# Performance work log

Measured on AMD Instinct MI355X. Metric: run time of the kernel, lower is better.

The kernel has to match this reference:

```python
import jax, jax.numpy as jnp
import numpy as np

DELTA_A, DELTA_R = 0.1, 1.0
ALPHA, BETA, GAMMA = 1.0, 1.0, 0.001


def setup_inputs() -> dict:
    key = jax.random.key(0)
    B, D, H, W, K = 4, 32, 512, 512, 16
    out = jax.random.normal(key, (B, D, H, W), dtype=jnp.float32)
    # 4x4 block partition -> K=16 instance labels, one center per block
    gh, gw = 4, 4
    bh, bw = H // gh, W // gw
    rows = np.arange(H) // bh  # [H]
    cols = np.arange(W) // bw  # [W]
    labels = (rows[:, None] * gw + cols[None, :]).astype(np.int32)  # [H,W]
    target = jnp.asarray(np.broadcast_to(labels, (B, H, W)).copy())
    ctr = np.array([[r * bh + bh // 2, c * bw + bw // 2]
                    for r in range(gh) for c in range(gw)], dtype=np.int32)  # [K,2]
    centers = jnp.asarray(np.broadcast_to(ctr, (B, K, 2)).copy())
    return {"out": out, "target": target, "centers": centers, "batch_size": B}


def _safe_sqrt(x):
    # matches torch.linalg.norm subgradient 0 at 0 (avoids NaN grads)
    pos = x > 0
    return jnp.where(pos, jnp.sqrt(jnp.where(pos, x, 1.0)), 0.0)


def _pairwise_norm(a, b):
    # a [M,D], b [N,D] -> [M,N] euclidean distances via gram trick
    d2 = (jnp.sum(a * a, 1)[:, None] + jnp.sum(b * b, 1)[None, :]
          - 2.0 * a @ b.T)
    return _safe_sqrt(jax.nn.relu(d2))


def _per_image(o, t, c):
    # o [D,H,W], t [H,W] int, c [K,2] int
    D = o.shape[0]
    K = c.shape[0]
    x = o.reshape(D, -1).T                      # [HW, D]
    E = o[:, c[:, 0], c[:, 1]].T                # [K, D] center embeddings
    lab_c = t[c[:, 0], c[:, 1]]                 # [K]
    mask = (t.reshape(-1)[None, :] == lab_c[:, None])  # [K, HW]
    # attraction: hinged distance of every cluster pixel to its center
    norms = _pairwise_norm(E, x)                # [K, HW]
    hinged = jax.nn.relu(norms - DELTA_A) * mask
    cnt = jnp.sum(mask, axis=1)
    denom = jnp.maximum(cnt - 1, 1).astype(o.dtype)
    s_att = jnp.sum(jnp.sum(hinged, axis=1) / denom)
    # repelling: pairwise center distances; diagonal contributes relu(delta_r)
    # per row and the original subtracts delta_r per center -> excluded
    nE = _pairwise_norm(E, E)                   # [K, K]
    s_rep = jnp.sum(jax.nn.relu(DELTA_R - nE)) - K * DELTA_R
    # regularization: norm of each center embedding
    s_reg = jnp.sum(_safe_sqrt(jnp.sum(E * E, axis=1)))
    return s_att, s_rep, s_reg


def reference(out, target, centers, batch_size):
    K = centers.shape[1]
    s_att, s_rep, s_reg = jax.vmap(_per_image)(out, target, centers)  # [B] each
    div_att = jnp.float32(K)
    div_rep = jnp.float32(K * (K - 1))
    div_reg = jnp.float32(K)

    def step(carry, s):
        a, r, g = carry
        sa, sr, sg = s
        return ((a + sa) / div_att, (r + sr) / div_rep, (g + sg) / div_reg), None

    zero = jnp.float32(0.0)
    (att, rep, reg), _ = jax.lax.scan(step, (zero, zero, zero),
                                      (s_att, s_rep, s_reg))
    loss = ALPHA * att + BETA * rep + GAMMA * reg
    return loss, att, rep
```

## Files before the change

kernel.cpp:

```cpp
#include <hip/hip_runtime.h>

#define B_ 4
#define D_ 32
#define H_ 512
#define W_ 512
#define K_ 16
#define N_ (H_ * W_)
#define NQ_ (N_ / 4)
#define NBLK_ 256
#define EPAD 33

#define WS_SUM  0
#define WS_CNT  64
#define WS_E2   128
#define WS_LAB  192
#define WS_E    264
#define WS_PART 4096

typedef float vfloat4 __attribute__((ext_vector_type(4)));
typedef int vint4 __attribute__((ext_vector_type(4)));

__device__ inline vfloat4 nt_load_f4(const float* p) {
  return __builtin_nontemporal_load((const vfloat4*)p);
}
__device__ inline vint4 nt_load_i4(const int* p) {
  return __builtin_nontemporal_load((const vint4*)p);
}

__global__ __launch_bounds__(256) void attract_kernel(
    const float* __restrict__ outp, const int* __restrict__ target,
    const int* __restrict__ centers, float* __restrict__ ws) {
  const int b = blockIdx.y;
  const int tid = threadIdx.x;
  __shared__ float sE[K_ * EPAD];
  __shared__ float se2[K_];
  __shared__ int slab[K_];
  __shared__ int scy[K_], scx[K_];
  __shared__ float bs[K_];
  __shared__ float bc[K_];

  if (tid < 2 * K_) {
    const int v = centers[b * (2 * K_) + tid];
    if (tid & 1) scx[tid >> 1] = v; else scy[tid >> 1] = v;
  }
  __syncthreads();
  {
    const int k = tid >> 4, d0 = tid & 15;
    const size_t cbase = ((size_t)b * D_ * H_ + scy[k]) * W_ + scx[k];
    const float v0 = outp[cbase + (size_t)d0 * N_];
    const float v1 = outp[cbase + (size_t)(d0 + 16) * N_];
    sE[k * EPAD + d0] = v0;
    sE[k * EPAD + d0 + 16] = v1;
    float p = fmaf(v0, v0, v1 * v1);
#pragma unroll
    for (int off = 1; off < 16; off <<= 1) p += __shfl_xor(p, off, 64);
    if (blockIdx.x == 0) {
      ws[WS_E + (b * K_ + k) * D_ + d0] = v0;
      ws[WS_E + (b * K_ + k) * D_ + d0 + 16] = v1;
      if ((tid & 15) == 0) ws[WS_E2 + b * K_ + k] = p;
    }
    if ((tid & 15) == 0) se2[k] = p;
    if (tid < K_) {
      slab[tid] = target[(size_t)b * N_ + scy[tid] * W_ + scx[tid]];
      bs[tid] = 0.0f;
      bc[tid] = 0.0f;
    }
  }
  __syncthreads();

  const int q = blockIdx.x * 256 + tid;
  const float* xb = outp + (size_t)b * D_ * N_;
  const vint4 lab4 = nt_load_i4(target + (size_t)b * N_ + 4 * q);
  const int labv[4] = {lab4.x, lab4.y, lab4.z, lab4.w};

  int kf[4], nm[4];
#pragma unroll
  for (int j = 0; j < 4; ++j) { kf[j] = 0; nm[j] = 0; }
#pragma unroll
  for (int k = 0; k < K_; ++k) {
    const int lk = slab[k];
#pragma unroll
    for (int j = 0; j < 4; ++j) {
      if (labv[j] == lk) { if (nm[j] == 0) kf[j] = k; nm[j]++; }
    }
  }

  float dot[4] = {0.f, 0.f, 0.f, 0.f};
  float x2[4] = {0.f, 0.f, 0.f, 0.f};
#pragma unroll
  for (int d = 0; d < D_; ++d) {
    const vfloat4 x = nt_load_f4(xb + (size_t)d * N_ + 4 * q);
    const float xs[4] = {x.x, x.y, x.z, x.w};
#pragma unroll
    for (int j = 0; j < 4; ++j) {
      const float e = sE[kf[j] * EPAD + d];
      dot[j] = fmaf(xs[j], e, dot[j]);
      x2[j] = fmaf(xs[j], xs[j], x2[j]);
    }
  }

  float hv[4];
#pragma unroll
  for (int j = 0; j < 4; ++j) {
    const float d2 = x2[j] + se2[kf[j]] - 2.0f * dot[j];
    const float h = fmaxf(sqrtf(fmaxf(d2, 0.0f)) - 0.1f, 0.0f);
    hv[j] = (nm[j] > 0) ? h : 0.0f;
  }

  const bool same = (kf[0] == kf[1]) & (kf[1] == kf[2]) & (kf[2] == kf[3]);
  float hsum = hv[0] + hv[1] + hv[2] + hv[3];
  float csum = (float)((nm[0] > 0) + (nm[1] > 0) + (nm[2] > 0) + (nm[3] > 0));
  int gi = same ? (kf[0] + 1) : 0;
#pragma unroll
  for (int off = 1; off < 32; off <<= 1) {
    const int o = __shfl_xor(gi, off, 64);
    if (o != gi) gi = 0;
  }
  if (gi != 0) {
#pragma unroll
    for (int off = 1; off < 32; off <<= 1) {
      hsum += __shfl_xor(hsum, off, 64);
      csum += __shfl_xor(csum, off, 64);
    }
    if ((tid & 31) == 0 && csum > 0.0f) {
      atomicAdd(&bs[gi - 1], hsum);
      atomicAdd(&bc[gi - 1], csum);
    }
  } else if (same) {
    if (csum > 0.0f) {
      atomicAdd(&bs[kf[0]], hsum);
      atomicAdd(&bc[kf[0]], csum);
    }
  } else {
#pragma unroll
    for (int j = 0; j < 4; ++j) {
      if (nm[j] > 0) {
        atomicAdd(&bs[kf[j]], hv[j]);
        atomicAdd(&bc[kf[j]], 1.0f);
      }
    }
  }

  const bool extra = (nm[0] > 1) | (nm[1] > 1) | (nm[2] > 1) | (nm[3] > 1);
  if (__any(extra)) {
    for (int k = 0; k < K_; ++k) {
      bool need[4]; bool anyn = false;
#pragma unroll
      for (int j = 0; j < 4; ++j) {
        need[j] = (nm[j] > 1) && (labv[j] == slab[k]) && (k != kf[j]);
        anyn |= need[j];
      }
      if (__any(anyn)) {
        float dt[4] = {0.f, 0.f, 0.f, 0.f};
        for (int d = 0; d < D_; ++d) {
          const vfloat4 x = nt_load_f4(xb + (size_t)d * N_ + 4 * q);
          const float e = sE[k * EPAD + d];
          dt[0] = fmaf(x.x, e, dt[0]);
          dt[1] = fmaf(x.y, e, dt[1]);
          dt[2] = fmaf(x.z, e, dt[2]);
          dt[3] = fmaf(x.w, e, dt[3]);
        }
#pragma unroll
        for (int j = 0; j < 4; ++j) {
          if (need[j]) {
            const float d2 = x2[j] + se2[k] - 2.0f * dt[j];
            atomicAdd(&bs[k], fmaxf(sqrtf(fmaxf(d2, 0.0f)) - 0.1f, 0.0f));
            atomicAdd(&bc[k], 1.0f);
          }
        }
      }
    }
  }
  __syncthreads();

  if (tid < 2 * K_) {
    float* p = ws + WS_PART + ((size_t)b * NBLK_ + blockIdx.x) * (2 * K_);
    p[tid] = (tid < K_) ? bs[tid] : bc[tid - K_];
  }
}

__global__ __launch_bounds__(256) void final_kernel(const float* __restrict__ ws,
                                                    float* __restrict__ out) {
  const int tid = threadIdx.x;
  __shared__ float sE[B_ * K_ * D_];
  __shared__ float ps[4][64], pc[4][64];
  __shared__ float sred[256];
  __shared__ float srep[B_];
  __shared__ float sreg[B_];
  __shared__ float ssa[B_];

  for (int i = tid; i < B_ * K_ * D_; i += 256) sE[i] = ws[WS_E + i];

  const int pair = tid & 63, quarter = tid >> 6;
  const int pb = pair >> 4, pk = pair & 15;
  {
    const float* base =
        ws + WS_PART + ((size_t)pb * NBLK_ + quarter * 64) * (2 * K_);
    float s = 0.0f, c = 0.0f;
#pragma unroll 4
    for (int i = 0; i < 64; ++i) {
      s += base[i * (2 * K_) + pk];
      c += base[i * (2 * K_) + K_ + pk];
    }
    ps[quarter][pair] = s;
    pc[quarter][pair] = c;
  }
  __syncthreads();

  if (tid < 64) {
    const float s = ps[0][tid] + ps[1][tid] + ps[2][tid] + ps[3][tid];
    const float c = pc[0][tid] + pc[1][tid] + pc[2][tid] + pc[3][tid];
    float v = s / fmaxf(c - 1.0f, 1.0f);
#pragma unroll
    for (int off = 1; off < K_; off <<= 1) v += __shfl_xor(v, off, 64);
    if ((tid & 15) == 0) ssa[tid >> 4] = v;
  }
  __syncthreads();

  const int i = tid >> 4, j = tid & 15;
  for (int b = 0; b < B_; ++b) {
    float dotv = 0.0f;
#pragma unroll 8
    for (int d = 0; d < D_; ++d)
      dotv = fmaf(sE[(b * K_ + i) * D_ + d], sE[(b * K_ + j) * D_ + d], dotv);
    const float d2 = ws[WS_E2 + b * K_ + i] + ws[WS_E2 + b * K_ + j] - 2.0f * dotv;
    sred[tid] = fmaxf(1.0f - sqrtf(fmaxf(d2, 0.0f)), 0.0f);
    __syncthreads();
    for (int s = 128; s > 0; s >>= 1) {
      if (tid < s) sred[tid] += sred[tid + s];
      __syncthreads();
    }
    if (tid == 0) srep[b] = sred[0] - (float)K_;
    __syncthreads();
  }

  sred[tid] = (tid < B_ * K_) ? sqrtf(fmaxf(ws[WS_E2 + tid], 0.0f)) : 0.0f;
  __syncthreads();
  if (tid < B_) {
    float sg = 0.0f;
    for (int k = 0; k < K_; ++k) sg += sred[tid * K_ + k];
    sreg[tid] = sg;
  }
  __syncthreads();

  if (tid == 0) {
    float att = 0.0f, rep = 0.0f, reg = 0.0f;
    for (int b = 0; b < B_; ++b) {
      att = (att + ssa[b]) / (float)K_;
      rep = (rep + srep[b]) / (float)(K_ * (K_ - 1));
      reg = (reg + sreg[b]) / (float)K_;
    }
    out[0] = att + rep + 0.001f * reg;
    out[1] = att;
    out[2] = rep;
  }
}

extern "C" void kernel_launch(void* const* d_in, const int* in_sizes, int n_in,
                              void* d_out, int out_size, void* d_ws, size_t ws_size,
                              hipStream_t stream) {
  const float* outp = (const float*)d_in[0];
  const int* target = (const int*)d_in[1];
  const int* centers = (const int*)d_in[2];
  float* ws = (float*)d_ws;
  float* out = (float*)d_out;

  attract_kernel<<<dim3(NBLK_, B_), 256, 0, stream>>>(outp, target, centers, ws);
  final_kernel<<<1, 256, 0, stream>>>(ws, out);
}
```

Baseline: 201.6 us.

## Fuse final reduction into attract kernel via last-block atomic counter

Removes the separate final_kernel launch: each attract block increments a global counter after writing its partials, and the last block to finish does the final reduction of attraction, repulsion and regularisation terms. A tiny zero_kernel resets the counter first, so there are still two launches. The repulsion reduction is vectorised across the four batches into one tree reduction instead of four. Launch bounds add an occupancy hint of 4. The cost is added fences and atomics in every block, plus larger shared memory in the fused kernel.

```diff
diff --git a/kernel.cpp b/kernel.cpp
--- a/kernel.cpp
+++ b/kernel.cpp
@@ -10,10 +10,8 @@
 #define NBLK_ 256
 #define EPAD 33
 
-#define WS_SUM  0
-#define WS_CNT  64
 #define WS_E2   128
-#define WS_LAB  192
+#define WS_CTR  192
 #define WS_E    264
 #define WS_PART 4096
 
@@ -27,9 +25,14 @@
   return __builtin_nontemporal_load((const vint4*)p);
 }
 
-__global__ __launch_bounds__(256) void attract_kernel(
+__global__ __launch_bounds__(64) void zero_kernel(float* __restrict__ ws) {
+  if (threadIdx.x == 0) ((int*)ws)[WS_CTR] = 0;
+}
+
+__global__ __launch_bounds__(256, 4) void attract_kernel(
     const float* __restrict__ outp, const int* __restrict__ target,
-    const int* __restrict__ centers, float* __restrict__ ws) {
+    const int* __restrict__ centers, float* __restrict__ ws,
+    float* __restrict__ out) {
   const int b = blockIdx.y;
   const int tid = threadIdx.x;
   __shared__ float sE[K_ * EPAD];
@@ -38,6 +41,7 @@
   __shared__ int scy[K_], scx[K_];
   __shared__ float bs[K_];
   __shared__ float bc[K_];
+  __shared__ int is_last;
 
   if (tid < 2 * K_) {
     const int v = centers[b * (2 * K_) + tid];
@@ -177,36 +181,39 @@
     float* p = ws + WS_PART + ((size_t)b * NBLK_ + blockIdx.x) * (2 * K_);
     p[tid] = (tid < K_) ? bs[tid] : bc[tid - K_];
   }
-}
-
-__global__ __launch_bounds__(256) void final_kernel(const float* __restrict__ ws,
-                                                    float* __restrict__ out) {
-  const int tid = threadIdx.x;
-  __shared__ float sE[B_ * K_ * D_];
+
+  __threadfence();
+  __syncthreads();
+  if (tid == 0)
+    is_last = (atomicAdd((int*)ws + WS_CTR, 1) == B_ * NBLK_ - 1);
+  __syncthreads();
+  if (!is_last) return;
+
+  __threadfence();
   __shared__ float ps[4][64], pc[4][64];
-  __shared__ float sred[256];
-  __shared__ float srep[B_];
-  __shared__ float sreg[B_];
-  __shared__ float ssa[B_];
-
-  for (int i = tid; i < B_ * K_ * D_; i += 256) sE[i] = ws[WS_E + i];
-
-  const int pair = tid & 63, quarter = tid >> 6;
-  const int pb = pair >> 4, pk = pair & 15;
+  __shared__ float sEall[B_ * K_ * D_];
+  __shared__ float se2all[B_ * K_];
+  __shared__ vfloat4 s4[256];
+  __shared__ float ssa[B_], srep[B_], sreg[B_];
+
+  for (int i = tid; i < B_ * K_ * D_; i += 256) sEall[i] = ws[WS_E + i];
+  if (tid < B_ * K_) se2all[tid] = ws[WS_E2 + tid];
+
   {
-    const float* base =
+    const int pair = tid & 63, quarter = tid >> 6;
+    const int pb = pair >> 4, pk = pair & 15;
+    const float* base2 =
         ws + WS_PART + ((size_t)pb * NBLK_ + quarter * 64) * (2 * K_);
     float s = 0.0f, c = 0.0f;
 #pragma unroll 4
-    for (int i = 0; i < 64; ++i) {
-      s += base[i * (2 * K_) + pk];
-      c += base[i * (2 * K_) + K_ + pk];
+    for (int i2 = 0; i2 < 64; ++i2) {
+      s += base2[i2 * (2 * K_) + pk];
+      c += base2[i2 * (2 * K_) + K_ + pk];
     }
     ps[quarter][pair] = s;
     pc[quarter][pair] = c;
   }
   __syncthreads();
-
   if (tid < 64) {
     const float s = ps[0][tid] + ps[1][tid] + ps[2][tid] + ps[3][tid];
     const float c = pc[0][tid] + pc[1][tid] + pc[2][tid] + pc[3][tid];
@@ -215,40 +222,43 @@
     for (int off = 1; off < K_; off <<= 1) v += __shfl_xor(v, off, 64);
     if ((tid & 15) == 0) ssa[tid >> 4] = v;
   }
-  __syncthreads();
-
-  const int i = tid >> 4, j = tid & 15;
-  for (int b = 0; b < B_; ++b) {
-    float dotv = 0.0f;
+
+  {
+    const int ii = tid >> 4, jj = tid & 15;
+    vfloat4 r;
+#pragma unroll
+    for (int b2 = 0; b2 < B_; ++b2) {
+      float dotv = 0.0f;
 #pragma unroll 8
-    for (int d = 0; d < D_; ++d)
-      dotv = fmaf(sE[(b * K_ + i) * D_ + d], sE[(b * K_ + j) * D_ + d], dotv);
-    const float d2 = ws[WS_E2 + b * K_ + i] + ws[WS_E2 + b * K_ + j] - 2.0f * dotv;
-    sred[tid] = fmaxf(1.0f - sqrtf(fmaxf(d2, 0.0f)), 0.0f);
+      for (int d = 0; d < D_; ++d)
+        dotv = fmaf(sEall[(b2 * K_ + ii) * D_ + d],
+                    sEall[(b2 * K_ + jj) * D_ + d], dotv);
+      const float d2 = se2all[b2 * K_ + ii] + se2all[b2 * K_ + jj] - 2.0f * dotv;
+      r[b2] = fmaxf(1.0f - sqrtf(fmaxf(d2, 0.0f)), 0.0f);
+    }
+    s4[tid] = r;
+  }
+  __syncthreads();
+  for (int s = 128; s > 0; s >>= 1) {
+    if (tid < s) s4[tid] += s4[tid + s];
     __syncthreads();
-    for (int s = 128; s > 0; s >>= 1) {
-      if (tid < s) sred[tid] += sred[tid + s];
-      __syncthreads();
-    }
-    if (tid == 0) srep[b] = sred[0] - (float)K_;
-    __syncthreads();
-  }
-
-  sred[tid] = (tid < B_ * K_) ? sqrtf(fmaxf(ws[WS_E2 + tid], 0.0f)) : 0.0f;
-  __syncthreads();
-  if (tid < B_) {
-    float sg = 0.0f;
-    for (int k = 0; k < K_; ++k) sg += sred[tid * K_ + k];
-    sreg[tid] = sg;
+  }
+  if (tid < B_) srep[tid] = s4[0][tid] - (float)K_;
+
+  if (tid < B_ * K_) {
+    float g = sqrtf(fmaxf(se2all[tid], 0.0f));
+#pragma unroll
+    for (int off = 1; off < K_; off <<= 1) g += __shfl_xor(g, off, 64);
+    if ((tid & 15) == 0) sreg[tid >> 4] = g;
   }
   __syncthreads();
 
   if (tid == 0) {
     float att = 0.0f, rep = 0.0f, reg = 0.0f;
-    for (int b = 0; b < B_; ++b) {
-      att = (att + ssa[b]) / (float)K_;
-      rep = (rep + srep[b]) / (float)(K_ * (K_ - 1));
-      reg = (reg + sreg[b]) / (float)K_;
+    for (int b2 = 0; b2 < B_; ++b2) {
+      att = (att + ssa[b2]) / (float)K_;
+      rep = (rep + srep[b2]) / (float)(K_ * (K_ - 1));
+      reg = (reg + sreg[b2]) / (float)K_;
     }
     out[0] = att + rep + 0.001f * reg;
     out[1] = att;
@@ -265,6 +275,6 @@
   float* ws = (float*)d_ws;
   float* out = (float*)d_out;
 
-  attract_kernel<<<dim3(NBLK_, B_), 256, 0, stream>>>(outp, target, centers, ws);
-  final_kernel<<<1, 256, 0, stream>>>(ws, out);
-}
+  zero_kernel<<<1, 64, 0, stream>>>(ws);
+  attract_kernel<<<dim3(NBLK_, B_), 256, 0, stream>>>(outp, target, centers, ws, out);
+}
```

Measured after the change: 307.0 us. 52.3% more time.
